# Optimization experiments

Measured on AMD Instinct MI355X. Metric: run time of the kernel, lower is better.

Reference implementation:

```python
import jax, jax.numpy as jnp
from jax import lax
import numpy as np


def setup_inputs() -> dict:
    key = jax.random.key(0)
    ks = jax.random.split(key, 10)
    B, C, T, H, W = 4, 128, 32, 24, 24
    M, k_t, k_s, mix_k = 3, 3, 3, 3
    s = 0.05
    q = jax.random.normal(ks[0], (B, C, T, H, W), jnp.float32)
    k = jax.random.normal(ks[1], (B, C, T, H, W), jnp.float32)
    v = jax.random.normal(ks[2], (B, C, T, H, W), jnp.float32)
    # depthwise 3D kernel banks: [M, C, 1, k_t, k_s, k_s] (OIDHW per branch, groups=C)
    Wk = jax.random.normal(ks[3], (M, C, 1, k_t, k_s, k_s), jnp.float32) * s
    Wv = jax.random.normal(ks[4], (M, C, 1, k_t, k_s, k_s), jnp.float32) * s
    # mix predictor: 1x1 conv1d (pointwise) + causal conv1d C->M
    pre_w = jax.random.normal(ks[5], (C, C), jnp.float32) * s
    pre_b = jax.random.normal(ks[6], (C,), jnp.float32) * s
    mix_w = jax.random.normal(ks[7], (M, C, mix_k), jnp.float32) * s
    mix_b = jax.random.normal(ks[8], (M,), jnp.float32) * s
    return {"q": q, "k": k, "v": v, "Wk": Wk, "Wv": Wv,
            "pre_w": pre_w, "pre_b": pre_b, "mix_w": mix_w, "mix_b": mix_b}


def _mix_alpha(q, pre_w, pre_b, mix_w, mix_b):
    # q: [B,C,T,H,W] -> global spatial pool -> [B,C,T]
    qg = q.mean(axis=(3, 4))
    h = jnp.einsum('oc,bct->bot', pre_w, qg) + pre_b[None, :, None]
    h = jax.nn.gelu(h, approximate=False)  # torch nn.GELU default = exact
    mix_k = mix_w.shape[-1]
    logits = lax.conv_general_dilated(
        h, mix_w, window_strides=(1,), padding=[(mix_k - 1, 0)],
        dimension_numbers=('NCH', 'OIH', 'NCH')) + mix_b[None, :, None]
    return jax.nn.softmax(logits, axis=1)  # [B,M,T]


def _dwconv3d_causal(x, w):
    # x: [B,C,T,H,W], w: [C,1,k_t,k_h,k_w] depthwise (groups=C)
    C = x.shape[1]
    k_t, k_h, k_w = w.shape[2], w.shape[3], w.shape[4]
    pad = [(k_t - 1, 0), (k_h // 2, k_h // 2), (k_w // 2, k_w // 2)]
    return lax.conv_general_dilated(
        x, w, window_strides=(1, 1, 1), padding=pad,
        dimension_numbers=('NCDHW', 'OIDHW', 'NCDHW'),
        feature_group_count=C)


def reference(q, k, v, Wk, Wv, pre_w, pre_b, mix_w, mix_b):
    alpha = _mix_alpha(q, pre_w, pre_b, mix_w, mix_b)  # [B,M,T]
    # all M depthwise branches at once: [M,B,C,T,H,W]
    km = jax.vmap(_dwconv3d_causal, in_axes=(None, 0))(k, Wk)
    vm = jax.vmap(_dwconv3d_causal, in_axes=(None, 0))(v, Wv)
    # per-time mixture-weighted sum over M
    k_out = jnp.einsum('mbcthw,bmt->bcthw', km, alpha)
    v_out = jnp.einsum('mbcthw,bmt->bcthw', vm, alpha)
    return (k_out, v_out)
```

## Files before the change

### kernel.cpp

```cpp
#include <hip/hip_runtime.h>
#include <math.h>

namespace {
constexpr int Bn = 4, Cn = 128, Tn = 32, Hn = 24, Wn = 24, Mn = 3;
constexpr int HWn = Hn * Wn;
constexpr int TTile = 16;
constexpr int PL = TTile + 2;
constexpr int RS = 28;
constexpr int PS = 26 * RS;
}

__global__ __launch_bounds__(256) void pool_kernel(const float* __restrict__ q,
                                                   float* __restrict__ qg) {
    int wave = threadIdx.x >> 6;
    int lane = threadIdx.x & 63;
    int plane = blockIdx.x * 4 + wave;
    const float4* p = (const float4*)(q + (size_t)plane * HWn);
    float4 a = p[lane];
    float4 b = p[lane + 64];
    float s = (a.x + a.y) + (a.z + a.w) + (b.x + b.y) + (b.z + b.w);
    if (lane < 16) {
        float4 c = p[128 + lane];
        s += (c.x + c.y) + (c.z + c.w);
    }
#pragma unroll
    for (int off = 32; off > 0; off >>= 1) s += __shfl_down(s, off);
    if (lane == 0) qg[plane] = s * (1.0f / 576.0f);
}

__global__ __launch_bounds__(512) void alpha_kernel(const float* __restrict__ qg,
                                                    const float* __restrict__ pre_w,
                                                    const float* __restrict__ pre_b,
                                                    const float* __restrict__ mix_w,
                                                    const float* __restrict__ mix_b,
                                                    float* __restrict__ alpha) {
    __shared__ float qg_s[Cn * Tn];
    __shared__ float h_s[Cn * (Tn + 2)];
    __shared__ float mw_s[Mn * Cn * 3];
    __shared__ float l_s[Mn * Tn];
    int b = blockIdx.x;
    int tid = threadIdx.x;
    for (int i = tid; i < Cn * Tn; i += 512) qg_s[i] = qg[b * Cn * Tn + i];
    for (int i = tid; i < Mn * Cn * 3; i += 512) mw_s[i] = mix_w[i];
    __syncthreads();
    {
        int o = tid >> 2;
        int t0 = (tid & 3) * 8;
        float bias = pre_b[o];
        float acc[8];
#pragma unroll
        for (int j = 0; j < 8; ++j) acc[j] = 0.f;
        const float* wrow = pre_w + o * Cn;
#pragma unroll 2
        for (int cb = 0; cb < Cn; cb += 8) {
            float wv[8];
#pragma unroll
            for (int j = 0; j < 8; ++j) wv[j] = wrow[cb + j];
#pragma unroll
            for (int j = 0; j < 8; ++j)
#pragma unroll
                for (int i = 0; i < 8; ++i)
                    acc[i] += wv[j] * qg_s[(cb + j) * Tn + t0 + i];
        }
        if ((tid & 3) == 0) { h_s[o * (Tn + 2) + 0] = 0.f; h_s[o * (Tn + 2) + 1] = 0.f; }
#pragma unroll
        for (int j = 0; j < 8; ++j) {
            float x = acc[j] + bias;
            h_s[o * (Tn + 2) + 2 + t0 + j] = 0.5f * x * (1.0f + erff(x * 0.70710678118654752f));
        }
    }
    __syncthreads();
    if (tid < Mn * Tn) {
        int m = tid / Tn, t = tid % Tn;
        float acc = mix_b[m];
#pragma unroll 8
        for (int c = 0; c < Cn; ++c) {
            const float* mw = mw_s + (m * Cn + c) * 3;
            const float* hp = h_s + c * (Tn + 2) + t;
            acc += mw[0] * hp[0] + mw[1] * hp[1] + mw[2] * hp[2];
        }
        l_s[m * Tn + t] = acc;
    }
    __syncthreads();
    if (tid < Tn) {
        int t = tid;
        float l0 = l_s[t], l1 = l_s[Tn + t], l2 = l_s[2 * Tn + t];
        float mx = fmaxf(l0, fmaxf(l1, l2));
        float e0 = expf(l0 - mx), e1 = expf(l1 - mx), e2 = expf(l2 - mx);
        float inv = 1.0f / (e0 + e1 + e2);
        alpha[(b * Mn + 0) * Tn + t] = e0 * inv;
        alpha[(b * Mn + 1) * Tn + t] = e1 * inv;
        alpha[(b * Mn + 2) * Tn + t] = e2 * inv;
    }
}

__global__ __launch_bounds__(384) void conv_kernel(const float* __restrict__ kin,
                                                   const float* __restrict__ vin,
                                                   const float* __restrict__ Wk,
                                                   const float* __restrict__ Wv,
                                                   const float* __restrict__ alpha,
                                                   float* __restrict__ out) {
    __shared__ float s[PL * PS];
    __shared__ float sw[TTile * 27];

    int bid = blockIdx.x;
    int tt = bid & 1;
    int c  = (bid >> 1) & 127;
    int b  = (bid >> 8) & 3;
    int br = bid >> 10;
    int t0 = tt * TTile;
    int tid = threadIdx.x;
    const size_t plane_base = (size_t)(b * Cn + c) * Tn;
    const float* __restrict__ src = br ? vin : kin;
    const float* __restrict__ Wb  = br ? Wv : Wk;

    for (int idx = tid; idx < PL * 26; idx += 384) {
        int p  = idx / 26;
        int rs = idx - p * 26;
        int tp = t0 - 2 + p;
        float4 g0, g1, g2, g3, g4, g5;
        bool valid = (tp >= 0) && ((unsigned)(rs - 1) < 24u);
        if (valid) {
            const float4* grow = (const float4*)(src + (plane_base + tp) * HWn + (rs - 1) * 24);
            g0 = grow[0]; g1 = grow[1]; g2 = grow[2];
            g3 = grow[3]; g4 = grow[4]; g5 = grow[5];
        } else {
            float4 z = make_float4(0.f, 0.f, 0.f, 0.f);
            g0 = z; g1 = z; g2 = z; g3 = z; g4 = z; g5 = z;
        }
        float4* dst = (float4*)(s + p * PS + rs * RS);
        dst[0] = make_float4(0.f,  g0.x, g0.y, g0.z);
        dst[1] = make_float4(g0.w, g1.x, g1.y, g1.z);
        dst[2] = make_float4(g1.w, g2.x, g2.y, g2.z);
        dst[3] = make_float4(g2.w, g3.x, g3.y, g3.z);
        dst[4] = make_float4(g3.w, g4.x, g4.y, g4.z);
        dst[5] = make_float4(g4.w, g5.x, g5.y, g5.z);
        dst[6] = make_float4(g5.w, 0.f,  0.f,  0.f);
    }
    for (int i = tid; i < TTile * 27; i += 384) {
        int tl = i / 27;
        int widx = i - tl * 27;
        float a0 = alpha[(b * Mn + 0) * Tn + t0 + tl];
        float a1 = alpha[(b * Mn + 1) * Tn + t0 + tl];
        float a2 = alpha[(b * Mn + 2) * Tn + t0 + tl];
        sw[i] = a0 * Wb[(0 * Cn + c) * 27 + widx]
              + a1 * Wb[(1 * Cn + c) * 27 + widx]
              + a2 * Wb[(2 * Cn + c) * 27 + widx];
    }
    __syncthreads();

    int tp8 = tid / 48;
    int rem = tid - tp8 * 48;
    int h = rem >> 1;
    int w0 = (rem & 1) * 12;
    int tl = tp8 * 2;
    const float* wp0 = sw + tl * 27;
    const float* wp1 = wp0 + 27;
    float acc0[12], acc1[12];
#pragma unroll
    for (int j = 0; j < 12; ++j) { acc0[j] = 0.f; acc1[j] = 0.f; }
#pragma unroll
    for (int p = 0; p < 4; ++p) {
        const float* pp = s + (tl + p) * PS;
#pragma unroll
        for (int dh = 0; dh < 3; ++dh) {
            const float* rp = pp + (h + dh) * RS + w0;
            float bf[14];
#pragma unroll
            for (int j = 0; j < 14; ++j) bf[j] = rp[j];
            if (p < 3) {
#pragma unroll
                for (int dw = 0; dw < 3; ++dw) {
                    float wc = wp0[p * 9 + dh * 3 + dw];
#pragma unroll
                    for (int j = 0; j < 12; ++j) acc0[j] += bf[j + dw] * wc;
                }
            }
            if (p >= 1) {
#pragma unroll
                for (int dw = 0; dw < 3; ++dw) {
                    float wc = wp1[(p - 1) * 9 + dh * 3 + dw];
#pragma unroll
                    for (int j = 0; j < 12; ++j) acc1[j] += bf[j + dw] * wc;
                }
            }
        }
    }
    size_t obase = (plane_base + t0 + tl) * HWn + h * Wn + w0;
    float* op = out + (br ? (size_t)Bn * Cn * Tn * HWn : 0) + obase;
#pragma unroll
    for (int j = 0; j < 3; ++j)
        ((float4*)op)[j] = make_float4(acc0[4*j], acc0[4*j+1], acc0[4*j+2], acc0[4*j+3]);
    op += HWn;
#pragma unroll
    for (int j = 0; j < 3; ++j)
        ((float4*)op)[j] = make_float4(acc1[4*j], acc1[4*j+1], acc1[4*j+2], acc1[4*j+3]);
}

extern "C" void kernel_launch(void* const* d_in, const int* in_sizes, int n_in,
                              void* d_out, int out_size, void* d_ws, size_t ws_size,
                              hipStream_t stream) {
    const float* q     = (const float*)d_in[0];
    const float* k     = (const float*)d_in[1];
    const float* v     = (const float*)d_in[2];
    const float* Wk    = (const float*)d_in[3];
    const float* Wv    = (const float*)d_in[4];
    const float* pre_w = (const float*)d_in[5];
    const float* pre_b = (const float*)d_in[6];
    const float* mix_w = (const float*)d_in[7];
    const float* mix_b = (const float*)d_in[8];
    float* out = (float*)d_out;

    float* qg    = (float*)d_ws;
    float* alpha = qg + Bn * Cn * Tn;

    hipLaunchKernelGGL(pool_kernel, dim3(Bn * Cn * Tn / 4), dim3(256), 0, stream, q, qg);
    hipLaunchKernelGGL(alpha_kernel, dim3(Bn), dim3(512), 0, stream,
                       qg, pre_w, pre_b, mix_w, mix_b, alpha);
    hipLaunchKernelGGL(conv_kernel, dim3(2 * Bn * Cn * (Tn / TTile)), dim3(384), 0, stream,
                       k, v, Wk, Wv, alpha, out);
}
```

Baseline: 212.2 us.

## Register-block two adjacent rows per thread and halve time tile in conv

The depthwise conv now gives each thread two adjacent output rows at a single time step instead of two time steps at a single row. The 27 mixed weights are preloaded into registers, and input rows are read from shared memory as float4 vectors. The time tile drops from 16 to 8 with 192-thread blocks, which doubles the grid and cuts shared memory per block. The aim is fewer LDS reads and scalar weight loads per FMA and higher occupancy, at the price of a larger halo overhead (10 planes loaded for 8 outputs).

```diff
diff --git a/kernel.cpp b/kernel.cpp
--- a/kernel.cpp
+++ b/kernel.cpp
@@ -4,10 +4,11 @@
 namespace {
 constexpr int Bn = 4, Cn = 128, Tn = 32, Hn = 24, Wn = 24, Mn = 3;
 constexpr int HWn = Hn * Wn;
-constexpr int TTile = 16;
+constexpr int TTile = 8;
 constexpr int PL = TTile + 2;
 constexpr int RS = 28;
 constexpr int PS = 26 * RS;
+constexpr int SWS = 28;
 }
 
 __global__ __launch_bounds__(256) void pool_kernel(const float* __restrict__ q,
@@ -94,27 +95,27 @@
     }
 }
 
-__global__ __launch_bounds__(384) void conv_kernel(const float* __restrict__ kin,
+__global__ __launch_bounds__(192) void conv_kernel(const float* __restrict__ kin,
                                                    const float* __restrict__ vin,
                                                    const float* __restrict__ Wk,
                                                    const float* __restrict__ Wv,
                                                    const float* __restrict__ alpha,
                                                    float* __restrict__ out) {
     __shared__ float s[PL * PS];
-    __shared__ float sw[TTile * 27];
+    __shared__ float sw[TTile * SWS];
 
     int bid = blockIdx.x;
-    int tt = bid & 1;
-    int c  = (bid >> 1) & 127;
-    int b  = (bid >> 8) & 3;
-    int br = bid >> 10;
+    int tt = bid & 3;
+    int c  = (bid >> 2) & 127;
+    int b  = (bid >> 9) & 3;
+    int br = bid >> 11;
     int t0 = tt * TTile;
     int tid = threadIdx.x;
     const size_t plane_base = (size_t)(b * Cn + c) * Tn;
     const float* __restrict__ src = br ? vin : kin;
     const float* __restrict__ Wb  = br ? Wv : Wk;
 
-    for (int idx = tid; idx < PL * 26; idx += 384) {
+    for (int idx = tid; idx < PL * 26; idx += 192) {
         int p  = idx / 26;
         int rs = idx - p * 26;
         int tp = t0 - 2 + p;
@@ -137,49 +138,63 @@
         dst[5] = make_float4(g4.w, g5.x, g5.y, g5.z);
         dst[6] = make_float4(g5.w, 0.f,  0.f,  0.f);
     }
-    for (int i = tid; i < TTile * 27; i += 384) {
+    for (int i = tid; i < TTile * 27; i += 192) {
         int tl = i / 27;
         int widx = i - tl * 27;
         float a0 = alpha[(b * Mn + 0) * Tn + t0 + tl];
         float a1 = alpha[(b * Mn + 1) * Tn + t0 + tl];
         float a2 = alpha[(b * Mn + 2) * Tn + t0 + tl];
-        sw[i] = a0 * Wb[(0 * Cn + c) * 27 + widx]
-              + a1 * Wb[(1 * Cn + c) * 27 + widx]
-              + a2 * Wb[(2 * Cn + c) * 27 + widx];
-    }
-    __syncthreads();
-
-    int tp8 = tid / 48;
-    int rem = tid - tp8 * 48;
-    int h = rem >> 1;
-    int w0 = (rem & 1) * 12;
-    int tl = tp8 * 2;
-    const float* wp0 = sw + tl * 27;
-    const float* wp1 = wp0 + 27;
+        sw[tl * SWS + widx] = a0 * Wb[(0 * Cn + c) * 27 + widx]
+                            + a1 * Wb[(1 * Cn + c) * 27 + widx]
+                            + a2 * Wb[(2 * Cn + c) * 27 + widx];
+    }
+    __syncthreads();
+
+    int tl   = tid / 24;
+    int rem  = tid - tl * 24;
+    int hp   = rem >> 1;
+    int half = rem & 1;
+    int h    = hp * 2;
+    int w0   = half * 12;
+    int cB4  = half * 12;
+
+    float wd[28];
+    {
+        const float4* wv = (const float4*)(sw + tl * SWS);
+#pragma unroll
+        for (int i = 0; i < 7; ++i) {
+            float4 t4 = wv[i];
+            wd[4*i+0] = t4.x; wd[4*i+1] = t4.y; wd[4*i+2] = t4.z; wd[4*i+3] = t4.w;
+        }
+    }
+
     float acc0[12], acc1[12];
 #pragma unroll
     for (int j = 0; j < 12; ++j) { acc0[j] = 0.f; acc1[j] = 0.f; }
 #pragma unroll
-    for (int p = 0; p < 4; ++p) {
+    for (int p = 0; p < 3; ++p) {
         const float* pp = s + (tl + p) * PS;
 #pragma unroll
-        for (int dh = 0; dh < 3; ++dh) {
-            const float* rp = pp + (h + dh) * RS + w0;
-            float bf[14];
-#pragma unroll
-            for (int j = 0; j < 14; ++j) bf[j] = rp[j];
-            if (p < 3) {
+        for (int r = 0; r < 4; ++r) {
+            const float* rp = pp + (h + r) * RS + cB4;
+            float bf[16];
+#pragma unroll
+            for (int cc = 0; cc < 4; ++cc) {
+                float4 t4 = *(const float4*)(rp + cc * 4);
+                bf[cc*4+0] = t4.x; bf[cc*4+1] = t4.y; bf[cc*4+2] = t4.z; bf[cc*4+3] = t4.w;
+            }
+            if (r < 3) {
 #pragma unroll
                 for (int dw = 0; dw < 3; ++dw) {
-                    float wc = wp0[p * 9 + dh * 3 + dw];
+                    float wc = wd[p * 9 + r * 3 + dw];
 #pragma unroll
                     for (int j = 0; j < 12; ++j) acc0[j] += bf[j + dw] * wc;
                 }
             }
-            if (p >= 1) {
+            if (r > 0) {
 #pragma unroll
                 for (int dw = 0; dw < 3; ++dw) {
-                    float wc = wp1[(p - 1) * 9 + dh * 3 + dw];
+                    float wc = wd[p * 9 + (r - 1) * 3 + dw];
 #pragma unroll
                     for (int j = 0; j < 12; ++j) acc1[j] += bf[j + dw] * wc;
                 }
@@ -191,7 +206,7 @@
 #pragma unroll
     for (int j = 0; j < 3; ++j)
         ((float4*)op)[j] = make_float4(acc0[4*j], acc0[4*j+1], acc0[4*j+2], acc0[4*j+3]);
-    op += HWn;
+    op += Wn;
 #pragma unroll
     for (int j = 0; j < 3; ++j)
         ((float4*)op)[j] = make_float4(acc1[4*j], acc1[4*j+1], acc1[4*j+2], acc1[4*j+3]);
@@ -217,6 +232,6 @@
     hipLaunchKernelGGL(pool_kernel, dim3(Bn * Cn * Tn / 4), dim3(256), 0, stream, q, qg);
     hipLaunchKernelGGL(alpha_kernel, dim3(Bn), dim3(512), 0, stream,
                        qg, pre_w, pre_b, mix_w, mix_b, alpha);
-    hipLaunchKernelGGL(conv_kernel, dim3(2 * Bn * Cn * (Tn / TTile)), dim3(384), 0, stream,
+    hipLaunchKernelGGL(conv_kernel, dim3(2 * Bn * Cn * (Tn / TTile)), dim3(192), 0, stream,
                        k, v, Wk, Wv, alpha, out);
 }
```

After: 210.7 us. About the same (-0.7%).
